# Optimization experiments

Measured on AMD Instinct MI355X. Metric: run time of the kernel, lower is better.

The kernel has to match this reference:

```python
import jax, jax.numpy as jnp
import numpy as np

N, KS, C = 1_000_000, 9, 16
EPS = 1e-5
SLOPE = 0.2  # LeakyReLU negative_slope


def _leaky(x):
    return jnp.where(x >= 0, x, SLOPE * x)


def _batchnorm(x, gamma, beta):
    # BatchNorm1d in training mode: biased batch statistics over the N axis
    mean = x.mean(axis=0)
    var = x.var(axis=0)
    return gamma * (x - mean) * jax.lax.rsqrt(var + EPS) + beta


def setup_inputs() -> dict:
    key = jax.random.key(0)
    k = jax.random.split(key, 5)
    xav = (2.0 / (C + C)) ** 0.5  # xavier-normal-ish scale for [C_in, C_out, ks]
    return {
        "data": jax.random.normal(k[0], (N, C), jnp.float32),
        "ind": jax.random.randint(k[1], (N, KS), 0, N),
        "w1": jax.random.normal(k[2], (C, C, KS), jnp.float32) * xav,
        "b1": jax.random.normal(k[3], (C,), jnp.float32) * 0.01,
        "gamma1": jnp.ones((C,), jnp.float32),
        "beta1": jnp.zeros((C,), jnp.float32),
        "w2": jax.random.normal(k[4], (C, C, KS), jnp.float32) * xav,
        "gamma2": jnp.ones((C,), jnp.float32),
        "beta2": jnp.zeros((C,), jnp.float32),
    }


def reference(data, ind, w1, b1, gamma1, beta1, w2, gamma2, beta2):
    # gather neighborhoods: [N, ks, C]
    inp = data[ind]
    # torch.einsum('ijk,klj->il', data[N,ks,C], weight[C,Cout,ks]) -> [N, Cout]
    out = jnp.einsum('njc,coj->no', inp, w1) + b1
    out = _leaky(_batchnorm(out, gamma1, beta1))
    # second gather + tree-conv, no bias
    out = jnp.einsum('njc,coj->no', out[ind], w2)
    out = _batchnorm(out, gamma2, beta2)
    # residual (in_channels == out_channels -> identity shortcut)
    return _leaky(out + data)
```

## Files before the change

### kernel.cpp

```cpp
#include <hip/hip_runtime.h>

typedef unsigned int uint;
typedef unsigned short ushort;

#define NN 1000000
#define KSZ 9
#define CH 16
#define KTOT 144
#define LSTR 168
#define NBLK 1024
#define TILES64 15625

typedef float f32x4 __attribute__((ext_vector_type(4)));
typedef short s16x8 __attribute__((ext_vector_type(8)));

__device__ __forceinline__ float bf2f(ushort v) { return __uint_as_float(((uint)v) << 16); }
__device__ __forceinline__ ushort f2bf(float f) {
  uint u = __float_as_uint(f);
  return (ushort)((u + 0x7fffu + ((u >> 16) & 1u)) >> 16);
}
__device__ __forceinline__ float leaky(float x) { return x >= 0.f ? x : 0.2f * x; }

template<bool SECOND>
__global__ __launch_bounds__(256)
void k_conv(const void* __restrict__ srcv, const int* __restrict__ ind,
            const float* __restrict__ w, const float* __restrict__ bias,
            const float* __restrict__ derived, ushort* __restrict__ outv,
            float* __restrict__ partial) {
  const int lane = threadIdx.x & 63;
  const int wid  = threadIdx.x >> 6;
  const int o = lane & 15;
  const int q = lane >> 4;

  __shared__ ushort lds[4][16 * LSTR];
  __shared__ float red[4][32];
  ushort* my = lds[wid];

  {
    int n = lane >> 2, part = lane & 3;
    *(unsigned long long*)&my[n * LSTR + KTOT + part * 4] = 0ULL;
  }

  s16x8 bfrag[5];
#pragma unroll
  for (int t = 0; t < 5; ++t) {
#pragma unroll
    for (int i = 0; i < 8; ++i) {
      int k = t * 32 + q * 8 + i;
      ushort wv = 0;
      if (k < KTOT) { int j = k >> 4, c = k & 15; wv = f2bf(w[(c * CH + o) * KSZ + j]); }
      bfrag[t][i] = (short)wv;
    }
  }

  float bo = 0.f;
  if (!SECOND) bo = bias[o];

  float sc[16], sh[16];
  if (SECOND) {
#pragma unroll
    for (int b = 0; b < 4; ++b) {
      float4 v = *(const float4*)(derived + b * 4);
      sc[b*4+0]=v.x; sc[b*4+1]=v.y; sc[b*4+2]=v.z; sc[b*4+3]=v.w;
      float4 u = *(const float4*)(derived + 16 + b * 4);
      sh[b*4+0]=u.x; sh[b*4+1]=u.y; sh[b*4+2]=u.z; sh[b*4+3]=u.w;
    }
  }

  float wsum = 0.f, wsq = 0.f;
  __syncthreads();

  for (int g = blockIdx.x; g < TILES64; g += NBLK) {
    const int base = g * 64 + wid * 16;
#pragma unroll
    for (int ph = 0; ph < 3; ++ph) {
      int r = lane + ph * 64;
      if (ph < 2 || lane < (KTOT - 128)) {
        int nsub = r / KSZ;
        int j = r - nsub * KSZ;
        int idx = ind[(base + nsub) * KSZ + j];
        uint pk[8];
        if (!SECOND) {
          const float4* sp = (const float4*)((const float*)srcv + (size_t)idx * CH);
          float4 f0 = sp[0], f1 = sp[1], f2 = sp[2], f3 = sp[3];
          float e[16] = {f0.x,f0.y,f0.z,f0.w, f1.x,f1.y,f1.z,f1.w,
                         f2.x,f2.y,f2.z,f2.w, f3.x,f3.y,f3.z,f3.w};
#pragma unroll
          for (int p = 0; p < 8; ++p)
            pk[p] = (uint)f2bf(e[2*p]) | ((uint)f2bf(e[2*p+1]) << 16);
        } else {
          const uint4* s4 = (const uint4*)((const ushort*)srcv + (size_t)idx * CH);
          uint4 lo = s4[0], hi = s4[1];
          uint uu[8] = {lo.x, lo.y, lo.z, lo.w, hi.x, hi.y, hi.z, hi.w};
#pragma unroll
          for (int p = 0; p < 8; ++p) {
            float e0 = __uint_as_float(uu[p] << 16);
            float e1 = __uint_as_float(uu[p] & 0xffff0000u);
            float x0 = leaky(sc[2*p] * e0 + sh[2*p]);
            float x1 = leaky(sc[2*p+1] * e1 + sh[2*p+1]);
            pk[p] = (uint)f2bf(x0) | ((uint)f2bf(x1) << 16);
          }
        }
        uint4* d4 = (uint4*)&my[nsub * LSTR + j * CH];
        d4[0] = *(uint4*)&pk[0];
        d4[1] = *(uint4*)&pk[4];
      }
    }
    __syncthreads();

    const ushort* ap = &my[o * LSTR + q * 8];
    f32x4 acc = {0.f, 0.f, 0.f, 0.f};
#pragma unroll
    for (int t = 0; t < 5; ++t) {
      s16x8 a = *(const s16x8*)(ap + t * 32);
      acc = __builtin_amdgcn_mfma_f32_16x16x32_bf16(a, bfrag[t], acc, 0, 0, 0);
    }
#pragma unroll
    for (int r = 0; r < 4; ++r) {
      float v = acc[r] + bo;
      ushort hv = f2bf(v);
      outv[(size_t)(base + q * 4 + r) * CH + o] = hv;
      float vr = bf2f(hv);
      wsum += vr;
      wsq  += vr * vr;
    }
    __syncthreads();
  }

  wsum += __shfl_xor(wsum, 16);  wsum += __shfl_xor(wsum, 32);
  wsq  += __shfl_xor(wsq, 16);   wsq  += __shfl_xor(wsq, 32);
  if (lane < 16) { red[wid][lane] = wsum; red[wid][16 + lane] = wsq; }
  __syncthreads();
  if (threadIdx.x < 32) {
    float s = red[0][threadIdx.x] + red[1][threadIdx.x] + red[2][threadIdx.x] + red[3][threadIdx.x];
    partial[blockIdx.x * 32 + threadIdx.x] = s;
  }
}

__global__ __launch_bounds__(256)
void k_finalize(const float* __restrict__ partial, const float* __restrict__ gamma,
                const float* __restrict__ beta, float* __restrict__ derived) {
  __shared__ float red[8][32];
  __shared__ float tot[32];
  int t = threadIdx.x, ch = t & 31, seg = t >> 5;
  float s = 0.f;
#pragma unroll 8
  for (int i = 0; i < 128; ++i) s += partial[(seg * 128 + i) * 32 + ch];
  red[seg][ch] = s;
  __syncthreads();
  if (t < 32) {
    float x = 0.f;
#pragma unroll
    for (int k = 0; k < 8; ++k) x += red[k][t];
    tot[t] = x;
  }
  __syncthreads();
  if (t < 16) {
    float mean = tot[t] * (1.0f / NN);
    float var  = tot[16 + t] * (1.0f / NN) - mean * mean;
    float scale = gamma[t] / sqrtf(var + 1e-5f);
    derived[t] = scale;
    derived[16 + t] = beta[t] - mean * scale;
  }
}

__global__ __launch_bounds__(256)
void k_final(const ushort* __restrict__ o2, const float* __restrict__ data,
             const float* __restrict__ drv, float* __restrict__ out) {
  size_t t = (size_t)blockIdx.x * 256 + threadIdx.x;
  size_t i0 = t * 8;
  if (i0 >= (size_t)NN * CH) return;
  int coff = (int)(i0 & 15);
  float4 s0 = *(const float4*)(drv + coff);
  float4 s1 = *(const float4*)(drv + coff + 4);
  float4 h0 = *(const float4*)(drv + 16 + coff);
  float4 h1 = *(const float4*)(drv + 16 + coff + 4);
  float sc[8] = {s0.x,s0.y,s0.z,s0.w,s1.x,s1.y,s1.z,s1.w};
  float sh[8] = {h0.x,h0.y,h0.z,h0.w,h1.x,h1.y,h1.z,h1.w};
  uint4 a = *(const uint4*)(o2 + i0);
  float4 d0 = *(const float4*)(data + i0);
  float4 d1 = *(const float4*)(data + i0 + 4);
  uint ua[4] = {a.x,a.y,a.z,a.w};
  float dd[8] = {d0.x,d0.y,d0.z,d0.w, d1.x,d1.y,d1.z,d1.w};
  float y[8];
#pragma unroll
  for (int p = 0; p < 4; ++p) {
    float x0 = __uint_as_float(ua[p] << 16);
    float x1 = __uint_as_float(ua[p] & 0xffff0000u);
    y[2*p]   = leaky(sc[2*p]   * x0 + sh[2*p]   + dd[2*p]);
    y[2*p+1] = leaky(sc[2*p+1] * x1 + sh[2*p+1] + dd[2*p+1]);
  }
  float4 r0 = {y[0], y[1], y[2], y[3]};
  float4 r1 = {y[4], y[5], y[6], y[7]};
  *(float4*)(out + i0) = r0;
  *(float4*)(out + i0 + 4) = r1;
}

extern "C" void kernel_launch(void* const* d_in, const int* in_sizes, int n_in,
                              void* d_out, int out_size, void* d_ws, size_t ws_size,
                              hipStream_t stream) {
  const float* data   = (const float*)d_in[0];
  const int*   ind    = (const int*)d_in[1];
  const float* w1     = (const float*)d_in[2];
  const float* b1     = (const float*)d_in[3];
  const float* gamma1 = (const float*)d_in[4];
  const float* beta1  = (const float*)d_in[5];
  const float* w2     = (const float*)d_in[6];
  const float* gamma2 = (const float*)d_in[7];
  const float* beta2  = (const float*)d_in[8];
  float* out = (float*)d_out;

  ushort* out1 = (ushort*)d_out;
  ushort* out2     = (ushort*)d_ws;
  float*  partial1 = (float*)((char*)d_ws + 32000000);
  float*  partial2 = partial1 + NBLK * 32;
  float*  derived1 = partial2 + NBLK * 32;
  float*  derived2 = derived1 + 32;

  hipLaunchKernelGGL((k_conv<false>), dim3(NBLK), dim3(256), 0, stream,
                     (const void*)data, ind, w1, b1, (const float*)nullptr, out1, partial1);
  hipLaunchKernelGGL(k_finalize, dim3(1), dim3(256), 0, stream,
                     partial1, gamma1, beta1, derived1);
  hipLaunchKernelGGL((k_conv<true>), dim3(NBLK), dim3(256), 0, stream,
                     (const void*)out1, ind, w2, (const float*)nullptr, derived1, out2, partial2);
  hipLaunchKernelGGL(k_finalize, dim3(1), dim3(256), 0, stream,
                     partial2, gamma2, beta2, derived2);
  hipLaunchKernelGGL(k_final, dim3((NN * CH / 8 + 255) / 256), dim3(256), 0, stream,
                     out2, data, derived2, out);
}
```

Before: 478.3 us.

## Precompute BN+leaky table once, drop per-gather transform and LDS barriers in conv

The first BatchNorm plus LeakyReLU moves into a separate elementwise kernel that writes a bf16 table once, so the second conv gathers already-transformed rows instead of redoing the affine and leaky work nine times per row. The per-tile __syncthreads barriers are removed because each wave only uses its own LDS slice. Index loads are hoisted ahead of the gathers, and the grid grows to 1792 blocks with a 7-waves occupancy hint. This adds an extra launch and a 32MB read/write pass. The LDS reuse without barriers depends on wave-local ordering being sufficient.

Result: slower. 489.4 us (+2.3%).

```diff
diff --git a/kernel.cpp b/kernel.cpp
--- a/kernel.cpp
+++ b/kernel.cpp
@@ -8,7 +8,7 @@
 #define CH 16
 #define KTOT 144
 #define LSTR 168
-#define NBLK 1024
+#define NBLK 1792
 #define TILES64 15625
 
 typedef float f32x4 __attribute__((ext_vector_type(4)));
@@ -21,12 +21,11 @@
 }
 __device__ __forceinline__ float leaky(float x) { return x >= 0.f ? x : 0.2f * x; }
 
-template<bool SECOND>
-__global__ __launch_bounds__(256)
+template<bool FP32SRC>
+__global__ __launch_bounds__(256, 7)
 void k_conv(const void* __restrict__ srcv, const int* __restrict__ ind,
             const float* __restrict__ w, const float* __restrict__ bias,
-            const float* __restrict__ derived, ushort* __restrict__ outv,
-            float* __restrict__ partial) {
+            ushort* __restrict__ outv, float* __restrict__ partial) {
   const int lane = threadIdx.x & 63;
   const int wid  = threadIdx.x >> 6;
   const int o = lane & 15;
@@ -53,34 +52,31 @@
     }
   }
 
-  float bo = 0.f;
-  if (!SECOND) bo = bias[o];
-
-  float sc[16], sh[16];
-  if (SECOND) {
-#pragma unroll
-    for (int b = 0; b < 4; ++b) {
-      float4 v = *(const float4*)(derived + b * 4);
-      sc[b*4+0]=v.x; sc[b*4+1]=v.y; sc[b*4+2]=v.z; sc[b*4+3]=v.w;
-      float4 u = *(const float4*)(derived + 16 + b * 4);
-      sh[b*4+0]=u.x; sh[b*4+1]=u.y; sh[b*4+2]=u.z; sh[b*4+3]=u.w;
-    }
-  }
-
+  float bo = FP32SRC ? bias[o] : 0.f;
   float wsum = 0.f, wsq = 0.f;
-  __syncthreads();
 
   for (int g = blockIdx.x; g < TILES64; g += NBLK) {
     const int base = g * 64 + wid * 16;
+
+    int idxv[3];
 #pragma unroll
     for (int ph = 0; ph < 3; ++ph) {
       int r = lane + ph * 64;
-      if (ph < 2 || lane < (KTOT - 128)) {
+      int rr = (r < KTOT) ? r : lane;
+      int nsub = rr / KSZ;
+      int j = rr - nsub * KSZ;
+      idxv[ph] = ind[(base + nsub) * KSZ + j];
+    }
+
+#pragma unroll
+    for (int ph = 0; ph < 3; ++ph) {
+      int r = lane + ph * 64;
+      if (r < KTOT) {
         int nsub = r / KSZ;
         int j = r - nsub * KSZ;
-        int idx = ind[(base + nsub) * KSZ + j];
+        int idx = idxv[ph];
         uint pk[8];
-        if (!SECOND) {
+        if (FP32SRC) {
           const float4* sp = (const float4*)((const float*)srcv + (size_t)idx * CH);
           float4 f0 = sp[0], f1 = sp[1], f2 = sp[2], f3 = sp[3];
           float e[16] = {f0.x,f0.y,f0.z,f0.w, f1.x,f1.y,f1.z,f1.w,
@@ -91,22 +87,14 @@
         } else {
           const uint4* s4 = (const uint4*)((const ushort*)srcv + (size_t)idx * CH);
           uint4 lo = s4[0], hi = s4[1];
-          uint uu[8] = {lo.x, lo.y, lo.z, lo.w, hi.x, hi.y, hi.z, hi.w};
-#pragma unroll
-          for (int p = 0; p < 8; ++p) {
-            float e0 = __uint_as_float(uu[p] << 16);
-            float e1 = __uint_as_float(uu[p] & 0xffff0000u);
-            float x0 = leaky(sc[2*p] * e0 + sh[2*p]);
-            float x1 = leaky(sc[2*p+1] * e1 + sh[2*p+1]);
-            pk[p] = (uint)f2bf(x0) | ((uint)f2bf(x1) << 16);
-          }
+          pk[0]=lo.x; pk[1]=lo.y; pk[2]=lo.z; pk[3]=lo.w;
+          pk[4]=hi.x; pk[5]=hi.y; pk[6]=hi.z; pk[7]=hi.w;
         }
         uint4* d4 = (uint4*)&my[nsub * LSTR + j * CH];
         d4[0] = *(uint4*)&pk[0];
         d4[1] = *(uint4*)&pk[4];
       }
     }
-    __syncthreads();
 
     const ushort* ap = &my[o * LSTR + q * 8];
     f32x4 acc = {0.f, 0.f, 0.f, 0.f};
@@ -124,7 +112,6 @@
       wsum += vr;
       wsq  += vr * vr;
     }
-    __syncthreads();
   }
 
   wsum += __shfl_xor(wsum, 16);  wsum += __shfl_xor(wsum, 32);
@@ -143,9 +130,9 @@
   __shared__ float red[8][32];
   __shared__ float tot[32];
   int t = threadIdx.x, ch = t & 31, seg = t >> 5;
+  const int PER = NBLK / 8;
   float s = 0.f;
-#pragma unroll 8
-  for (int i = 0; i < 128; ++i) s += partial[(seg * 128 + i) * 32 + ch];
+  for (int i = 0; i < PER; ++i) s += partial[(seg * PER + i) * 32 + ch];
   red[seg][ch] = s;
   __syncthreads();
   if (t < 32) {
@@ -162,6 +149,34 @@
     derived[t] = scale;
     derived[16 + t] = beta[t] - mean * scale;
   }
+}
+
+__global__ __launch_bounds__(256)
+void k_bnleaky(const ushort* __restrict__ in, const float* __restrict__ drv,
+               ushort* __restrict__ outp) {
+  size_t t = (size_t)blockIdx.x * 256 + threadIdx.x;
+  size_t i0 = t * 8;
+  if (i0 >= (size_t)NN * CH) return;
+  int coff = (int)(i0 & 15);
+  float4 s0 = *(const float4*)(drv + coff);
+  float4 s1 = *(const float4*)(drv + coff + 4);
+  float4 h0 = *(const float4*)(drv + 16 + coff);
+  float4 h1 = *(const float4*)(drv + 16 + coff + 4);
+  float sc[8] = {s0.x,s0.y,s0.z,s0.w,s1.x,s1.y,s1.z,s1.w};
+  float sh[8] = {h0.x,h0.y,h0.z,h0.w,h1.x,h1.y,h1.z,h1.w};
+  uint4 a = *(const uint4*)(in + i0);
+  uint ua[4] = {a.x,a.y,a.z,a.w};
+  uint res[4];
+#pragma unroll
+  for (int p = 0; p < 4; ++p) {
+    float x0 = __uint_as_float(ua[p] << 16);
+    float x1 = __uint_as_float(ua[p] & 0xffff0000u);
+    float y0 = leaky(sc[2*p]   * x0 + sh[2*p]);
+    float y1 = leaky(sc[2*p+1] * x1 + sh[2*p+1]);
+    res[p] = (uint)f2bf(y0) | ((uint)f2bf(y1) << 16);
+  }
+  uint4 r4; r4.x=res[0]; r4.y=res[1]; r4.z=res[2]; r4.w=res[3];
+  *(uint4*)(outp + i0) = r4;
 }
 
 __global__ __launch_bounds__(256)
@@ -211,20 +226,25 @@
   float* out = (float*)d_out;
 
   ushort* out1 = (ushort*)d_out;
+  ushort* htab = (ushort*)d_out + (size_t)NN * CH;
   ushort* out2     = (ushort*)d_ws;
   float*  partial1 = (float*)((char*)d_ws + 32000000);
   float*  partial2 = partial1 + NBLK * 32;
   float*  derived1 = partial2 + NBLK * 32;
   float*  derived2 = derived1 + 32;
 
-  hipLaunchKernelGGL((k_conv<false>), dim3(NBLK), dim3(256), 0, stream,
-                     (const void*)data, ind, w1, b1, (const float*)nullptr, out1, partial1);
+  const int EBLK = (NN * CH / 8 + 255) / 256;
+
+  hipLaunchKernelGGL((k_conv<true>), dim3(NBLK), dim3(256), 0, stream,
+                     (const void*)data, ind, w1, b1, out1, partial1);
   hipLaunchKernelGGL(k_finalize, dim3(1), dim3(256), 0, stream,
                      partial1, gamma1, beta1, derived1);
-  hipLaunchKernelGGL((k_conv<true>), dim3(NBLK), dim3(256), 0, stream,
-                     (const void*)out1, ind, w2, (const float*)nullptr, derived1, out2, partial2);
+  hipLaunchKernelGGL(k_bnleaky, dim3(EBLK), dim3(256), 0, stream,
+                     out1, derived1, htab);
+  hipLaunchKernelGGL((k_conv<false>), dim3(NBLK), dim3(256), 0, stream,
+                     (const void*)htab, ind, w2, (const float*)nullptr, out2, partial2);
   hipLaunchKernelGGL(k_finalize, dim3(1), dim3(256), 0, stream,
                      partial2, gamma2, beta2, derived2);
-  hipLaunchKernelGGL(k_final, dim3((NN * CH / 8 + 255) / 256), dim3(256), 0, stream,
+  hipLaunchKernelGGL(k_final, dim3(EBLK), dim3(256), 0, stream,
                      out2, data, derived2, out);
 }
```

## Drop block barriers in conv, prefetch gather indices, widen finalize reduction

Applied to the files above, without the earlier changes.

The conv kernel no longer calls __syncthreads around each tile, since each wavefront writes and reads only its own LDS slice. It also loads all three neighbour indices before issuing the gathers so the index loads overlap. The finalize kernel now runs with 1024 threads and explicit 8-way unrolled loads to shorten its serial reduction. Without barriers, correctness relies on wavefront-level LDS ordering; there is no explicit wave barrier between the cross-lane LDS writes and the MFMA reads, so this could race.

New measurement: 475.0 us. No clear change (-0.7%).

```diff
diff --git a/kernel.cpp b/kernel.cpp
--- a/kernel.cpp
+++ b/kernel.cpp
@@ -21,7 +21,7 @@
 }
 __device__ __forceinline__ float leaky(float x) { return x >= 0.f ? x : 0.2f * x; }
 
-template<bool SECOND>
+template<bool FP32SRC>
 __global__ __launch_bounds__(256)
 void k_conv(const void* __restrict__ srcv, const int* __restrict__ ind,
             const float* __restrict__ w, const float* __restrict__ bias,
@@ -53,11 +53,10 @@
     }
   }
 
-  float bo = 0.f;
-  if (!SECOND) bo = bias[o];
+  float bo = FP32SRC ? bias[o] : 0.f;
 
   float sc[16], sh[16];
-  if (SECOND) {
+  if (!FP32SRC) {
 #pragma unroll
     for (int b = 0; b < 4; ++b) {
       float4 v = *(const float4*)(derived + b * 4);
@@ -68,19 +67,29 @@
   }
 
   float wsum = 0.f, wsq = 0.f;
-  __syncthreads();
 
   for (int g = blockIdx.x; g < TILES64; g += NBLK) {
     const int base = g * 64 + wid * 16;
+
+    int idxv[3];
 #pragma unroll
     for (int ph = 0; ph < 3; ++ph) {
       int r = lane + ph * 64;
-      if (ph < 2 || lane < (KTOT - 128)) {
+      int rr = (r < KTOT) ? r : lane;
+      int nsub = rr / KSZ;
+      int j = rr - nsub * KSZ;
+      idxv[ph] = ind[(base + nsub) * KSZ + j];
+    }
+
+#pragma unroll
+    for (int ph = 0; ph < 3; ++ph) {
+      int r = lane + ph * 64;
+      if (r < KTOT) {
         int nsub = r / KSZ;
         int j = r - nsub * KSZ;
-        int idx = ind[(base + nsub) * KSZ + j];
+        int idx = idxv[ph];
         uint pk[8];
-        if (!SECOND) {
+        if (FP32SRC) {
           const float4* sp = (const float4*)((const float*)srcv + (size_t)idx * CH);
           float4 f0 = sp[0], f1 = sp[1], f2 = sp[2], f3 = sp[3];
           float e[16] = {f0.x,f0.y,f0.z,f0.w, f1.x,f1.y,f1.z,f1.w,
@@ -106,7 +115,6 @@
         d4[1] = *(uint4*)&pk[4];
       }
     }
-    __syncthreads();
 
     const ushort* ap = &my[o * LSTR + q * 8];
     f32x4 acc = {0.f, 0.f, 0.f, 0.f};
@@ -124,7 +132,6 @@
       wsum += vr;
       wsq  += vr * vr;
     }
-    __syncthreads();
   }
 
   wsum += __shfl_xor(wsum, 16);  wsum += __shfl_xor(wsum, 32);
@@ -137,21 +144,31 @@
   }
 }
 
-__global__ __launch_bounds__(256)
+__global__ __launch_bounds__(1024)
 void k_finalize(const float* __restrict__ partial, const float* __restrict__ gamma,
                 const float* __restrict__ beta, float* __restrict__ derived) {
-  __shared__ float red[8][32];
+  __shared__ float red[32][33];
   __shared__ float tot[32];
   int t = threadIdx.x, ch = t & 31, seg = t >> 5;
   float s = 0.f;
-#pragma unroll 8
-  for (int i = 0; i < 128; ++i) s += partial[(seg * 128 + i) * 32 + ch];
+#pragma unroll
+  for (int i = 0; i < 32; i += 8) {
+    float a0 = partial[(seg * 32 + i + 0) * 32 + ch];
+    float a1 = partial[(seg * 32 + i + 1) * 32 + ch];
+    float a2 = partial[(seg * 32 + i + 2) * 32 + ch];
+    float a3 = partial[(seg * 32 + i + 3) * 32 + ch];
+    float a4 = partial[(seg * 32 + i + 4) * 32 + ch];
+    float a5 = partial[(seg * 32 + i + 5) * 32 + ch];
+    float a6 = partial[(seg * 32 + i + 6) * 32 + ch];
+    float a7 = partial[(seg * 32 + i + 7) * 32 + ch];
+    s += ((a0 + a1) + (a2 + a3)) + ((a4 + a5) + (a6 + a7));
+  }
   red[seg][ch] = s;
   __syncthreads();
   if (t < 32) {
     float x = 0.f;
 #pragma unroll
-    for (int k = 0; k < 8; ++k) x += red[k][t];
+    for (int k = 0; k < 32; ++k) x += red[k][t];
     tot[t] = x;
   }
   __syncthreads();
@@ -217,13 +234,13 @@
   float*  derived1 = partial2 + NBLK * 32;
   float*  derived2 = derived1 + 32;
 
+  hipLaunchKernelGGL((k_conv<true>), dim3(NBLK), dim3(256), 0, stream,
+                     (const void*)data, ind, w1, b1, (const float*)nullptr, out1, partial1);
+  hipLaunchKernelGGL(k_finalize, dim3(1), dim3(1024), 0, stream,
+                     partial1, gamma1, beta1, derived1);
   hipLaunchKernelGGL((k_conv<false>), dim3(NBLK), dim3(256), 0, stream,
-                     (const void*)data, ind, w1, b1, (const float*)nullptr, out1, partial1);
-  hipLaunchKernelGGL(k_finalize, dim3(1), dim3(256), 0, stream,
-                     partial1, gamma1, beta1, derived1);
-  hipLaunchKernelGGL((k_conv<true>), dim3(NBLK), dim3(256), 0, stream,
                      (const void*)out1, ind, w2, (const float*)nullptr, derived1, out2, partial2);
-  hipLaunchKernelGGL(k_finalize, dim3(1), dim3(256), 0, stream,
+  hipLaunchKernelGGL(k_finalize, dim3(1), dim3(1024), 0, stream,
                      partial2, gamma2, beta2, derived2);
   hipLaunchKernelGGL(k_final, dim3((NN * CH / 8 + 255) / 256), dim3(256), 0, stream,
                      out2, data, derived2, out);
```
